# Optimization experiments

Measured on AMD Instinct MI355X. Metric: run time of the kernel, lower is better.

The kernel has to match this reference:

```python
import jax, jax.numpy as jnp
import numpy as np

SEQ, IN_DIM, OUT_DIM = 8192, 1024, 1024

def setup_inputs() -> dict:
    key = jax.random.key(0)
    k1, k2, k3, k4 = jax.random.split(key, 4)
    inputs = jax.random.normal(k1, (SEQ, IN_DIM), dtype=jnp.float32)
    # torch.nn.Linear stores weight as [out_dim, in_dim]; y = x @ W.T
    w_query = jax.random.normal(k2, (OUT_DIM, IN_DIM), dtype=jnp.float32) * (1.0 / np.sqrt(IN_DIM))
    w_key = jax.random.normal(k3, (OUT_DIM, IN_DIM), dtype=jnp.float32) * (1.0 / np.sqrt(IN_DIM))
    w_value = jax.random.normal(k4, (OUT_DIM, IN_DIM), dtype=jnp.float32) * (1.0 / np.sqrt(IN_DIM))
    return {"inputs": inputs, "w_query": w_query, "w_key": w_key, "w_value": w_value}

def reference(inputs, w_query, w_key, w_value):
    # QKV projections: [S, D_out]
    q = inputs @ w_query.T
    k = inputs @ w_key.T
    v = inputs @ w_value.T
    scale = 1.0 / jnp.sqrt(jnp.asarray(k.shape[-1], dtype=q.dtype))
    scores = (q @ k.T) * scale  # [S, S]
    # causal mask: lower-triangular kept, upper set to -inf
    s = scores.shape[0]
    causal = jnp.tril(jnp.ones((s, s), dtype=bool))
    scores = jnp.where(causal, scores, -jnp.inf)
    attn = jax.nn.softmax(scores, axis=-1)
    return attn @ v
```

## Files before the change

kernel.cpp:

```cpp
#include <hip/hip_runtime.h>
#include <stdint.h>
#include <stddef.h>


#define SEQ   8192
#define DIM   1024

typedef __bf16 bf16x8 __attribute__((ext_vector_type(8)));
typedef float  f32x4  __attribute__((ext_vector_type(4)));

#define MFMA16(a, b, c) __builtin_amdgcn_mfma_f32_16x16x32_bf16((a), (b), (c), 0, 0, 0)

__device__ __forceinline__ uint16_t f2bf(float f) {
  uint32_t u = __builtin_bit_cast(uint32_t, f);
  return (uint16_t)((u + 0x7fffu + ((u >> 16) & 1u)) >> 16);
}
__device__ __forceinline__ float bf2f(uint16_t h) {
  uint32_t u = ((uint32_t)h) << 16;
  return __builtin_bit_cast(float, u);
}

typedef const __attribute__((address_space(1))) uint32_t* gas_t;
typedef __attribute__((address_space(3))) uint32_t* las_t;
__device__ __forceinline__ void async16(const void* g, void* l) {
  __builtin_amdgcn_global_load_lds((gas_t)g, (las_t)l, 16, 0, 0);
}

__global__ __launch_bounds__(256) void cast_all(const float* __restrict__ x,
                                                const float* __restrict__ wq,
                                                const float* __restrict__ wk,
                                                const float* __restrict__ wv,
                                                uint16_t* __restrict__ xb,
                                                uint16_t* __restrict__ wcat) {
  int b = blockIdx.x;
  const float* src;
  uint16_t* dst;
  int i;
  if (b < 8192) {
    src = x; dst = xb; i = (b * 256 + threadIdx.x) * 4;
  } else {
    int wb = b - 8192;
    int sel = wb >> 10;
    src = sel == 0 ? wq : (sel == 1 ? wk : wv);
    dst = wcat + sel * 1048576;
    i = ((wb & 1023) * 256 + threadIdx.x) * 4;
  }
  float4 v = *(const float4*)(src + i);
  ushort4 o;
  o.x = f2bf(v.x); o.y = f2bf(v.y); o.z = f2bf(v.z); o.w = f2bf(v.w);
  *(ushort4*)(dst + i) = o;
}

__global__ __launch_bounds__(256) void qkv_gemm(const uint16_t* __restrict__ A,
                                                const uint16_t* __restrict__ B,
                                                uint16_t* __restrict__ Qblk,
                                                uint16_t* __restrict__ Kblk,
                                                uint16_t* __restrict__ Vblk) {
  __shared__ __align__(16) uint16_t As[128 * 64];
  __shared__ __align__(16) uint16_t Bs[128 * 64];
  const int t    = threadIdx.x;
  const int w    = t >> 6;
  const int lane = t & 63;
  const int lm   = lane & 15;
  const int qd   = lane >> 4;
  const int wrow = (w >> 1) * 64;
  const int wcol = (w & 1) * 64;
  const int rowbase = blockIdx.y * 128;
  const int colbase = blockIdx.x * 128;

  const int lrow = lane >> 3;
  const int lgrp = (lane & 7) ^ (lrow & 7);

  f32x4 acc[4][4] = {};

  for (int kb = 0; kb < DIM; kb += 64) {
    __syncthreads();
#pragma unroll
    for (int rep = 0; rep < 4; ++rep) {
      int r0 = rep * 32 + w * 8;
      async16(A + (size_t)(rowbase + r0 + lrow) * DIM + kb + lgrp * 8, As + r0 * 64);
      async16(B + (size_t)(colbase + r0 + lrow) * DIM + kb + lgrp * 8, Bs + r0 * 64);
    }
    __syncthreads();
#pragma unroll
    for (int kc = 0; kc < 2; ++kc) {
      bf16x8 af[4], bfr[4];
#pragma unroll
      for (int mt = 0; mt < 4; ++mt) {
        int r = wrow + mt * 16 + lm;
        af[mt] = *(const bf16x8*)(As + r * 64 + (((kc * 4 + qd) ^ (lm & 7)) * 8));
      }
#pragma unroll
      for (int nt = 0; nt < 4; ++nt) {
        int r = wcol + nt * 16 + lm;
        bfr[nt] = *(const bf16x8*)(Bs + r * 64 + (((kc * 4 + qd) ^ (lm & 7)) * 8));
      }
#pragma unroll
      for (int mt = 0; mt < 4; ++mt)
#pragma unroll
        for (int nt = 0; nt < 4; ++nt)
          acc[mt][nt] = MFMA16(af[mt], bfr[nt], acc[mt][nt]);
    }
  }

#pragma unroll
  for (int mt = 0; mt < 4; ++mt)
#pragma unroll
    for (int nt = 0; nt < 4; ++nt)
#pragma unroll
      for (int r = 0; r < 4; ++r) {
        int m = rowbase + wrow + mt * 16 + qd * 4 + r;
        int n = colbase + wcol + nt * 16 + lm;
        uint16_t v = f2bf(acc[mt][nt][r]);
        int nn = n & 1023;
        if (n < 2048) {
          size_t off = (((size_t)(m >> 4) * 32 + (nn >> 5)) * 64 +
                        ((nn >> 3) & 3) * 16 + (m & 15)) * 8 + (nn & 7);
          if (n < 1024) Qblk[off] = v; else Kblk[off] = v;
        } else {
          size_t off = (((size_t)(nn >> 4) * 256 + (m >> 5)) * 64 +
                        ((m >> 3) & 3) * 16 + (nn & 15)) * 8 + (m & 7);
          Vblk[off] = v;
        }
      }
}

__global__ __launch_bounds__(512, 2) void attn_kernel(const uint16_t* __restrict__ Qblk,
                                                      const uint16_t* __restrict__ Kblk,
                                                      const uint16_t* __restrict__ Vblk,
                                                      uint16_t* __restrict__ P0,
                                                      uint16_t* __restrict__ P1,
                                                      float* __restrict__ Mm,
                                                      float* __restrict__ Ll) {
  __shared__ __align__(16) uint16_t Qs[32768];
  __shared__ __align__(16) uint16_t Pb[8192];
  __shared__ float stats[32][8];
  __shared__ float mrow[32];

  const int t    = threadIdx.x;
  const int w    = t >> 6;
  const int lane = t & 63;
  const int lm   = lane & 15;
  const int qd   = lane >> 4;
  const int par  = blockIdx.x & 1;
  const int p    = blockIdx.x >> 1;
  const float c1 = 0.045084220027780106f;

#pragma unroll 1
  for (int half = 0; half < 2; ++half) {
    const int tt   = half ? 255 - p : p;
    const int row0 = tt * 32;
    const int jn   = (tt >> 3) + 1;

    __syncthreads();
#pragma unroll
    for (int i = 0; i < 8; ++i)
      async16(Qblk + ((size_t)(tt * 64 + w * 8 + i)) * 512 + lane * 8,
              Qs + (w * 8 + i) * 512);

    bf16x8 kpre0[4], kpre1[4];
    {
      const uint16_t* kbp0 = Kblk + ((size_t)(par * 16 + w * 2) * 32) * 512 + lane * 8;
#pragma unroll
      for (int c = 0; c < 4; ++c) {
        kpre0[c] = *(const bf16x8*)(kbp0 + (size_t)c * 512);
        kpre1[c] = *(const bf16x8*)(kbp0 + (size_t)(32 + c) * 512);
      }
    }
    __syncthreads();

    float m_run[2][4], l_run[2][4];
#pragma unroll
    for (int mt = 0; mt < 2; ++mt)
#pragma unroll
      for (int r = 0; r < 4; ++r) { m_run[mt][r] = -1e30f; l_run[mt][r] = 0.0f; }
    f32x4 o_acc[2][8] = {};

#pragma unroll 1
    for (int jg = par; jg < jn; jg += 2) {
      const uint16_t* kbp = Kblk + ((size_t)(jg * 16 + w * 2) * 32) * 512 + lane * 8;
      const uint16_t* vbp = Vblk + ((size_t)(w * 8) * 256 + jg * 8) * 512 + lane * 8;
      const uint16_t* qsp = Qs + lane * 8;

      f32x4 sacc[2][2] = {};
      bf16x8 kr0[8], kr1[8];
#pragma unroll
      for (int c = 0; c < 4; ++c) { kr0[c] = kpre0[c]; kr1[c] = kpre1[c]; }
#pragma unroll
      for (int c = 4; c < 8; ++c) {
        kr0[c] = *(const bf16x8*)(kbp + (size_t)c * 512);
        kr1[c] = *(const bf16x8*)(kbp + (size_t)(32 + c) * 512);
      }
#pragma unroll
      for (int kb = 0; kb < 32; ++kb) {
        bf16x8 q0 = *(const bf16x8*)(qsp + kb * 512);
        bf16x8 q1 = *(const bf16x8*)(qsp + (32 + kb) * 512);
        sacc[0][0] = MFMA16(q0, kr0[kb & 7], sacc[0][0]);
        sacc[1][0] = MFMA16(q1, kr0[kb & 7], sacc[1][0]);
        sacc[0][1] = MFMA16(q0, kr1[kb & 7], sacc[0][1]);
        sacc[1][1] = MFMA16(q1, kr1[kb & 7], sacc[1][1]);
        if (kb < 24) {
          kr0[kb & 7] = *(const bf16x8*)(kbp + (size_t)(kb + 8) * 512);
          kr1[kb & 7] = *(const bf16x8*)(kbp + (size_t)(32 + kb + 8) * 512);
        }
      }

      if (jg == jn - 1) {
#pragma unroll
        for (int mt = 0; mt < 2; ++mt)
#pragma unroll
          for (int nt = 0; nt < 2; ++nt)
#pragma unroll
            for (int r = 0; r < 4; ++r) {
              int col = jg * 256 + w * 32 + nt * 16 + lm;
              int row = row0 + mt * 16 + qd * 4 + r;
              if (col > row) sacc[mt][nt][r] = -1e30f;
            }
      }

#pragma unroll
      for (int mt = 0; mt < 2; ++mt)
#pragma unroll
        for (int r = 0; r < 4; ++r) {
          float v = fmaxf(sacc[mt][0][r], sacc[mt][1][r]);
          v = fmaxf(v, __shfl_xor(v, 1));
          v = fmaxf(v, __shfl_xor(v, 2));
          v = fmaxf(v, __shfl_xor(v, 4));
          v = fmaxf(v, __shfl_xor(v, 8));
          if (lm == 0) stats[mt * 16 + qd * 4 + r][w] = v;
        }
      __syncthreads();

      bf16x8 vr0[8], vr1[8];
#pragma unroll
      for (int dt = 0; dt < 8; ++dt) {
        vr0[dt] = *(const bf16x8*)(vbp + ((size_t)dt * 256 + 0) * 512);
        vr1[dt] = *(const bf16x8*)(vbp + ((size_t)dt * 256 + 1) * 512);
      }

      float alpha[2][4], psum[2][4];
#pragma unroll
      for (int mt = 0; mt < 2; ++mt)
#pragma unroll
        for (int r = 0; r < 4; ++r) {
          int rl = mt * 16 + qd * 4 + r;
          float4 g0 = *(const float4*)&stats[rl][0];
          float4 g1 = *(const float4*)&stats[rl][4];
          float gm = fmaxf(fmaxf(fmaxf(g0.x, g0.y), fmaxf(g0.z, g0.w)),
                           fmaxf(fmaxf(g1.x, g1.y), fmaxf(g1.z, g1.w)));
          float mn = fmaxf(m_run[mt][r], gm);
          alpha[mt][r] = exp2f((m_run[mt][r] - mn) * c1);
          m_run[mt][r] = mn;
          psum[mt][r] = 0.0f;
        }
#pragma unroll
      for (int mt = 0; mt < 2; ++mt)
#pragma unroll
        for (int nt = 0; nt < 2; ++nt)
#pragma unroll
          for (int r = 0; r < 4; ++r) {
            float pv = exp2f((sacc[mt][nt][r] - m_run[mt][r]) * c1);
            psum[mt][r] += pv;
            Pb[((mt * 8 + w) * 64 + (nt * 2 + (lm >> 3)) * 16 + qd * 4 + r) * 8 +
               (lm & 7)] = f2bf(pv);
          }
#pragma unroll
      for (int mt = 0; mt < 2; ++mt)
#pragma unroll
        for (int r = 0; r < 4; ++r) {
          float s2 = psum[mt][r];
          s2 += __shfl_xor(s2, 1);
          s2 += __shfl_xor(s2, 2);
          s2 += __shfl_xor(s2, 4);
          s2 += __shfl_xor(s2, 8);
          l_run[mt][r] = l_run[mt][r] * alpha[mt][r] + s2;
        }
      __syncthreads();

      {
        const uint16_t* kbpn = Kblk + ((size_t)((jg + 2) * 16 + w * 2) * 32) * 512 + lane * 8;
#pragma unroll
        for (int c = 0; c < 4; ++c) {
          kpre0[c] = *(const bf16x8*)(kbpn + (size_t)c * 512);
          kpre1[c] = *(const bf16x8*)(kbpn + (size_t)(32 + c) * 512);
        }
      }

#pragma unroll
      for (int mt = 0; mt < 2; ++mt)
#pragma unroll
        for (int dt = 0; dt < 8; ++dt)
#pragma unroll
          for (int r = 0; r < 4; ++r)
            o_acc[mt][dt][r] *= alpha[mt][r];

#pragma unroll
      for (int kc = 0; kc < 8; ++kc) {
        bf16x8 pf0 = *(const bf16x8*)(Pb + (kc * 64 + lane) * 8);
        bf16x8 pf1 = *(const bf16x8*)(Pb + ((8 + kc) * 64 + lane) * 8);
#pragma unroll
        for (int dt = 0; dt < 8; ++dt) {
          bf16x8 vf = (kc & 1) ? vr1[dt] : vr0[dt];
          o_acc[0][dt] = MFMA16(pf0, vf, o_acc[0][dt]);
          o_acc[1][dt] = MFMA16(pf1, vf, o_acc[1][dt]);
        }
        if (kc < 6) {
#pragma unroll
          for (int dt = 0; dt < 8; ++dt) {
            if (kc & 1)
              vr1[dt] = *(const bf16x8*)(vbp + ((size_t)dt * 256 + kc + 2) * 512);
            else
              vr0[dt] = *(const bf16x8*)(vbp + ((size_t)dt * 256 + kc + 2) * 512);
          }
        }
      }
    }

    if (lm == 0) {
#pragma unroll
      for (int mt = 0; mt < 2; ++mt)
#pragma unroll
        for (int r = 0; r < 4; ++r) {
          int rl = mt * 16 + qd * 4 + r;
          stats[rl][w] = l_run[mt][r];
          if (w == 0) mrow[rl] = m_run[mt][r];
        }
    }
    __syncthreads();
    if (t < 32) {
      float4 a0 = *(const float4*)&stats[t][0];
      float4 a1 = *(const float4*)&stats[t][4];
      Mm[par * SEQ + row0 + t] = mrow[t];
      Ll[par * SEQ + row0 + t] = (a0.x + a0.y + a0.z + a0.w) + (a1.x + a1.y + a1.z + a1.w);
    }
    uint16_t* Pp = par ? P1 : P0;
#pragma unroll
    for (int mt = 0; mt < 2; ++mt)
#pragma unroll
      for (int dt = 0; dt < 8; ++dt)
#pragma unroll
        for (int r = 0; r < 4; ++r) {
          int row = row0 + mt * 16 + qd * 4 + r;
          int d   = w * 128 + dt * 16 + lm;
          Pp[(size_t)row * DIM + d] = f2bf(o_acc[mt][dt][r]);
        }
  }
}

__global__ __launch_bounds__(256) void merge_kernel(const uint16_t* __restrict__ P0,
                                                    const uint16_t* __restrict__ P1,
                                                    const float* __restrict__ Mm,
                                                    const float* __restrict__ Ll,
                                                    float* __restrict__ out) {
  const int row = blockIdx.x;
  const int d0  = threadIdx.x * 4;
  const float c1 = 0.045084220027780106f;
  float m0 = Mm[row], m1 = Mm[SEQ + row];
  float l0 = Ll[row], l1 = Ll[SEQ + row];
  float m  = fmaxf(m0, m1);
  float a0 = exp2f((m0 - m) * c1);
  float a1 = exp2f((m1 - m) * c1);
  float inv = 1.0f / (a0 * l0 + a1 * l1);
  ushort4 p0 = *(const ushort4*)(P0 + (size_t)row * DIM + d0);
  ushort4 p1 = *(const ushort4*)(P1 + (size_t)row * DIM + d0);
  float4 o;
  o.x = (a0 * bf2f(p0.x) + a1 * bf2f(p1.x)) * inv;
  o.y = (a0 * bf2f(p0.y) + a1 * bf2f(p1.y)) * inv;
  o.z = (a0 * bf2f(p0.z) + a1 * bf2f(p1.z)) * inv;
  o.w = (a0 * bf2f(p0.w) + a1 * bf2f(p1.w)) * inv;
  *(float4*)(out + (size_t)row * DIM + d0) = o;
}

extern "C" void kernel_launch(void* const* d_in, const int* in_sizes, int n_in,
                              void* d_out, int out_size, void* d_ws, size_t ws_size,
                              hipStream_t stream) {
  (void)in_sizes; (void)n_in; (void)out_size; (void)ws_size;
  const float* x  = (const float*)d_in[0];
  const float* wq = (const float*)d_in[1];
  const float* wk = (const float*)d_in[2];
  const float* wv = (const float*)d_in[3];
  float* out = (float*)d_out;

  char* ws = (char*)d_ws;
  uint16_t* Qblk = (uint16_t*)(ws);
  uint16_t* Kblk = (uint16_t*)(ws + 16777216);
  uint16_t* Vblk = (uint16_t*)(ws + 33554432);
  uint16_t* P0   = (uint16_t*)(ws + 50331648);
  uint16_t* xb   = (uint16_t*)(ws + 67108864);
  uint16_t* P1   = (uint16_t*)(ws + 67108864);
  uint16_t* wcat = (uint16_t*)(ws + 83886080);
  float*    Mm   = (float*)(ws + 83886080);
  float*    Ll   = (float*)(ws + 83886080 + 65536);

  cast_all<<<11264, 256, 0, stream>>>(x, wq, wk, wv, xb, wcat);
  qkv_gemm<<<dim3(24, 64), 256, 0, stream>>>(xb, wcat, Qblk, Kblk, Vblk);
  attn_kernel<<<256, 512, 0, stream>>>(Qblk, Kblk, Vblk, P0, P1, Mm, Ll);
  merge_kernel<<<SEQ, 256, 0, stream>>>(P0, P1, Mm, Ll, out);
}
```

Before: 532.5 us.

## Launch one attention block per query tile and alias softmax stats into P buffer

The attention kernel no longer processes two query tiles (p and 255-p) in a loop per block. It now launches 512 blocks, each handling one tile and one key parity, and raises the launch-bounds occupancy hint from 2 to 4. The row-max and row-sum scratch arrays now reuse the P staging buffer in shared memory, which needs extra barriers. This aims for more concurrency and less idle time per block. The cost is losing the balanced pairing of light and heavy causal tiles, and the tighter register budget risks spills.

```diff
diff --git a/kernel.cpp b/kernel.cpp
--- a/kernel.cpp
+++ b/kernel.cpp
@@ -125,7 +125,7 @@
       }
 }
 
-__global__ __launch_bounds__(512, 2) void attn_kernel(const uint16_t* __restrict__ Qblk,
+__global__ __launch_bounds__(512, 4) void attn_kernel(const uint16_t* __restrict__ Qblk,
                                                       const uint16_t* __restrict__ Kblk,
                                                       const uint16_t* __restrict__ Vblk,
                                                       uint16_t* __restrict__ P0,
@@ -134,217 +134,224 @@
                                                       float* __restrict__ Ll) {
   __shared__ __align__(16) uint16_t Qs[32768];
   __shared__ __align__(16) uint16_t Pb[8192];
-  __shared__ float stats[32][8];
-  __shared__ float mrow[32];
+  float* const stats = (float*)Pb;
+  float* const mrow  = (float*)Pb + 256;
 
   const int t    = threadIdx.x;
   const int w    = t >> 6;
   const int lane = t & 63;
   const int lm   = lane & 15;
   const int qd   = lane >> 4;
-  const int par  = blockIdx.x & 1;
-  const int p    = blockIdx.x >> 1;
+  const int b    = blockIdx.x;
+  const int pi   = b >> 1;
+  const int par  = b & 1;
+  const int tt   = par ? 255 - pi : pi;
+  const int row0 = tt * 32;
+  const int jn   = (tt >> 3) + 1;
   const float c1 = 0.045084220027780106f;
 
+#pragma unroll
+  for (int i = 0; i < 8; ++i)
+    async16(Qblk + ((size_t)(tt * 64 + w * 8 + i)) * 512 + lane * 8,
+            Qs + (w * 8 + i) * 512);
+
+  bf16x8 kpre0[4], kpre1[4];
+  {
+    const uint16_t* kbp0 = Kblk + ((size_t)(par * 16 + w * 2) * 32) * 512 + lane * 8;
+#pragma unroll
+    for (int c = 0; c < 4; ++c) {
+      kpre0[c] = *(const bf16x8*)(kbp0 + (size_t)c * 512);
+      kpre1[c] = *(const bf16x8*)(kbp0 + (size_t)(32 + c) * 512);
+    }
+  }
+  __syncthreads();
+
+  float m_run[2][4], l_run[2][4];
+#pragma unroll
+  for (int mt = 0; mt < 2; ++mt)
+#pragma unroll
+    for (int r = 0; r < 4; ++r) { m_run[mt][r] = -1e30f; l_run[mt][r] = 0.0f; }
+  f32x4 o_acc[2][8] = {};
+
 #pragma unroll 1
-  for (int half = 0; half < 2; ++half) {
-    const int tt   = half ? 255 - p : p;
-    const int row0 = tt * 32;
-    const int jn   = (tt >> 3) + 1;
-
-    __syncthreads();
-#pragma unroll
-    for (int i = 0; i < 8; ++i)
-      async16(Qblk + ((size_t)(tt * 64 + w * 8 + i)) * 512 + lane * 8,
-              Qs + (w * 8 + i) * 512);
-
-    bf16x8 kpre0[4], kpre1[4];
+  for (int jg = par; jg < jn; jg += 2) {
+    const uint16_t* kbp = Kblk + ((size_t)(jg * 16 + w * 2) * 32) * 512 + lane * 8;
+    const uint16_t* vbp = Vblk + ((size_t)(w * 8) * 256 + jg * 8) * 512 + lane * 8;
+    const uint16_t* qsp = Qs + lane * 8;
+
+    f32x4 sacc[2][2] = {};
+    bf16x8 kr0[8], kr1[8];
+#pragma unroll
+    for (int c = 0; c < 4; ++c) { kr0[c] = kpre0[c]; kr1[c] = kpre1[c]; }
+#pragma unroll
+    for (int c = 4; c < 8; ++c) {
+      kr0[c] = *(const bf16x8*)(kbp + (size_t)c * 512);
+      kr1[c] = *(const bf16x8*)(kbp + (size_t)(32 + c) * 512);
+    }
+#pragma unroll
+    for (int kb = 0; kb < 32; ++kb) {
+      bf16x8 q0 = *(const bf16x8*)(qsp + kb * 512);
+      bf16x8 q1 = *(const bf16x8*)(qsp + (32 + kb) * 512);
+      sacc[0][0] = MFMA16(q0, kr0[kb & 7], sacc[0][0]);
+      sacc[1][0] = MFMA16(q1, kr0[kb & 7], sacc[1][0]);
+      sacc[0][1] = MFMA16(q0, kr1[kb & 7], sacc[0][1]);
+      sacc[1][1] = MFMA16(q1, kr1[kb & 7], sacc[1][1]);
+      if (kb < 24) {
+        kr0[kb & 7] = *(const bf16x8*)(kbp + (size_t)(kb + 8) * 512);
+        kr1[kb & 7] = *(const bf16x8*)(kbp + (size_t)(32 + kb + 8) * 512);
+      }
+    }
+
+    if (jg == jn - 1) {
+#pragma unroll
+      for (int mt = 0; mt < 2; ++mt)
+#pragma unroll
+        for (int nt = 0; nt < 2; ++nt)
+#pragma unroll
+          for (int r = 0; r < 4; ++r) {
+            int col = jg * 256 + w * 32 + nt * 16 + lm;
+            int row = row0 + mt * 16 + qd * 4 + r;
+            if (col > row) sacc[mt][nt][r] = -1e30f;
+          }
+    }
+
+    float rmax[2][4];
+#pragma unroll
+    for (int mt = 0; mt < 2; ++mt)
+#pragma unroll
+      for (int r = 0; r < 4; ++r) {
+        float v = fmaxf(sacc[mt][0][r], sacc[mt][1][r]);
+        v = fmaxf(v, __shfl_xor(v, 1));
+        v = fmaxf(v, __shfl_xor(v, 2));
+        v = fmaxf(v, __shfl_xor(v, 4));
+        v = fmaxf(v, __shfl_xor(v, 8));
+        rmax[mt][r] = v;
+      }
+    __syncthreads();
+
+#pragma unroll
+    for (int mt = 0; mt < 2; ++mt)
+#pragma unroll
+      for (int r = 0; r < 4; ++r)
+        if (lm == 0) stats[(mt * 16 + qd * 4 + r) * 8 + w] = rmax[mt][r];
+    __syncthreads();
+
+    float alpha[2][4], psum[2][4];
+#pragma unroll
+    for (int mt = 0; mt < 2; ++mt)
+#pragma unroll
+      for (int r = 0; r < 4; ++r) {
+        int rl = mt * 16 + qd * 4 + r;
+        float4 g0 = *(const float4*)&stats[rl * 8];
+        float4 g1 = *(const float4*)&stats[rl * 8 + 4];
+        float gm = fmaxf(fmaxf(fmaxf(g0.x, g0.y), fmaxf(g0.z, g0.w)),
+                         fmaxf(fmaxf(g1.x, g1.y), fmaxf(g1.z, g1.w)));
+        float mn = fmaxf(m_run[mt][r], gm);
+        alpha[mt][r] = exp2f((m_run[mt][r] - mn) * c1);
+        m_run[mt][r] = mn;
+        psum[mt][r] = 0.0f;
+      }
+    __syncthreads();
+
+    bf16x8 vr0[8], vr1[8];
+#pragma unroll
+    for (int dt = 0; dt < 8; ++dt) {
+      vr0[dt] = *(const bf16x8*)(vbp + ((size_t)dt * 256 + 0) * 512);
+      vr1[dt] = *(const bf16x8*)(vbp + ((size_t)dt * 256 + 1) * 512);
+    }
+
+#pragma unroll
+    for (int mt = 0; mt < 2; ++mt)
+#pragma unroll
+      for (int nt = 0; nt < 2; ++nt)
+#pragma unroll
+        for (int r = 0; r < 4; ++r) {
+          float pv = exp2f((sacc[mt][nt][r] - m_run[mt][r]) * c1);
+          psum[mt][r] += pv;
+          Pb[((mt * 8 + w) * 64 + (nt * 2 + (lm >> 3)) * 16 + qd * 4 + r) * 8 +
+             (lm & 7)] = f2bf(pv);
+        }
+#pragma unroll
+    for (int mt = 0; mt < 2; ++mt)
+#pragma unroll
+      for (int r = 0; r < 4; ++r) {
+        float s2 = psum[mt][r];
+        s2 += __shfl_xor(s2, 1);
+        s2 += __shfl_xor(s2, 2);
+        s2 += __shfl_xor(s2, 4);
+        s2 += __shfl_xor(s2, 8);
+        l_run[mt][r] = l_run[mt][r] * alpha[mt][r] + s2;
+      }
+    __syncthreads();
+
     {
-      const uint16_t* kbp0 = Kblk + ((size_t)(par * 16 + w * 2) * 32) * 512 + lane * 8;
+      const uint16_t* kbpn = Kblk + ((size_t)((jg + 2) * 16 + w * 2) * 32) * 512 + lane * 8;
 #pragma unroll
       for (int c = 0; c < 4; ++c) {
-        kpre0[c] = *(const bf16x8*)(kbp0 + (size_t)c * 512);
-        kpre1[c] = *(const bf16x8*)(kbp0 + (size_t)(32 + c) * 512);
-      }
-    }
-    __syncthreads();
-
-    float m_run[2][4], l_run[2][4];
-#pragma unroll
-    for (int mt = 0; mt < 2; ++mt)
-#pragma unroll
-      for (int r = 0; r < 4; ++r) { m_run[mt][r] = -1e30f; l_run[mt][r] = 0.0f; }
-    f32x4 o_acc[2][8] = {};
-
-#pragma unroll 1
-    for (int jg = par; jg < jn; jg += 2) {
-      const uint16_t* kbp = Kblk + ((size_t)(jg * 16 + w * 2) * 32) * 512 + lane * 8;
-      const uint16_t* vbp = Vblk + ((size_t)(w * 8) * 256 + jg * 8) * 512 + lane * 8;
-      const uint16_t* qsp = Qs + lane * 8;
-
-      f32x4 sacc[2][2] = {};
-      bf16x8 kr0[8], kr1[8];
-#pragma unroll
-      for (int c = 0; c < 4; ++c) { kr0[c] = kpre0[c]; kr1[c] = kpre1[c]; }
-#pragma unroll
-      for (int c = 4; c < 8; ++c) {
-        kr0[c] = *(const bf16x8*)(kbp + (size_t)c * 512);
-        kr1[c] = *(const bf16x8*)(kbp + (size_t)(32 + c) * 512);
-      }
-#pragma unroll
-      for (int kb = 0; kb < 32; ++kb) {
-        bf16x8 q0 = *(const bf16x8*)(qsp + kb * 512);
-        bf16x8 q1 = *(const bf16x8*)(qsp + (32 + kb) * 512);
-        sacc[0][0] = MFMA16(q0, kr0[kb & 7], sacc[0][0]);
-        sacc[1][0] = MFMA16(q1, kr0[kb & 7], sacc[1][0]);
-        sacc[0][1] = MFMA16(q0, kr1[kb & 7], sacc[0][1]);
-        sacc[1][1] = MFMA16(q1, kr1[kb & 7], sacc[1][1]);
-        if (kb < 24) {
-          kr0[kb & 7] = *(const bf16x8*)(kbp + (size_t)(kb + 8) * 512);
-          kr1[kb & 7] = *(const bf16x8*)(kbp + (size_t)(32 + kb + 8) * 512);
+        kpre0[c] = *(const bf16x8*)(kbpn + (size_t)c * 512);
+        kpre1[c] = *(const bf16x8*)(kbpn + (size_t)(32 + c) * 512);
+      }
+    }
+
+#pragma unroll
+    for (int mt = 0; mt < 2; ++mt)
+#pragma unroll
+      for (int dt = 0; dt < 8; ++dt)
+#pragma unroll
+        for (int r = 0; r < 4; ++r)
+          o_acc[mt][dt][r] *= alpha[mt][r];
+
+#pragma unroll
+    for (int kc = 0; kc < 8; ++kc) {
+      bf16x8 pf0 = *(const bf16x8*)(Pb + (kc * 64 + lane) * 8);
+      bf16x8 pf1 = *(const bf16x8*)(Pb + ((8 + kc) * 64 + lane) * 8);
+#pragma unroll
+      for (int dt = 0; dt < 8; ++dt) {
+        bf16x8 vf = (kc & 1) ? vr1[dt] : vr0[dt];
+        o_acc[0][dt] = MFMA16(pf0, vf, o_acc[0][dt]);
+        o_acc[1][dt] = MFMA16(pf1, vf, o_acc[1][dt]);
+      }
+      if (kc < 6) {
+#pragma unroll
+        for (int dt = 0; dt < 8; ++dt) {
+          if (kc & 1)
+            vr1[dt] = *(const bf16x8*)(vbp + ((size_t)dt * 256 + kc + 2) * 512);
+          else
+            vr0[dt] = *(const bf16x8*)(vbp + ((size_t)dt * 256 + kc + 2) * 512);
         }
       }
-
-      if (jg == jn - 1) {
-#pragma unroll
-        for (int mt = 0; mt < 2; ++mt)
-#pragma unroll
-          for (int nt = 0; nt < 2; ++nt)
-#pragma unroll
-            for (int r = 0; r < 4; ++r) {
-              int col = jg * 256 + w * 32 + nt * 16 + lm;
-              int row = row0 + mt * 16 + qd * 4 + r;
-              if (col > row) sacc[mt][nt][r] = -1e30f;
-            }
-      }
-
-#pragma unroll
-      for (int mt = 0; mt < 2; ++mt)
-#pragma unroll
-        for (int r = 0; r < 4; ++r) {
-          float v = fmaxf(sacc[mt][0][r], sacc[mt][1][r]);
-          v = fmaxf(v, __shfl_xor(v, 1));
-          v = fmaxf(v, __shfl_xor(v, 2));
-          v = fmaxf(v, __shfl_xor(v, 4));
-          v = fmaxf(v, __shfl_xor(v, 8));
-          if (lm == 0) stats[mt * 16 + qd * 4 + r][w] = v;
-        }
-      __syncthreads();
-
-      bf16x8 vr0[8], vr1[8];
-#pragma unroll
-      for (int dt = 0; dt < 8; ++dt) {
-        vr0[dt] = *(const bf16x8*)(vbp + ((size_t)dt * 256 + 0) * 512);
-        vr1[dt] = *(const bf16x8*)(vbp + ((size_t)dt * 256 + 1) * 512);
-      }
-
-      float alpha[2][4], psum[2][4];
-#pragma unroll
-      for (int mt = 0; mt < 2; ++mt)
-#pragma unroll
-        for (int r = 0; r < 4; ++r) {
-          int rl = mt * 16 + qd * 4 + r;
-          float4 g0 = *(const float4*)&stats[rl][0];
-          float4 g1 = *(const float4*)&stats[rl][4];
-          float gm = fmaxf(fmaxf(fmaxf(g0.x, g0.y), fmaxf(g0.z, g0.w)),
-                           fmaxf(fmaxf(g1.x, g1.y), fmaxf(g1.z, g1.w)));
-          float mn = fmaxf(m_run[mt][r], gm);
-          alpha[mt][r] = exp2f((m_run[mt][r] - mn) * c1);
-          m_run[mt][r] = mn;
-          psum[mt][r] = 0.0f;
-        }
-#pragma unroll
-      for (int mt = 0; mt < 2; ++mt)
-#pragma unroll
-        for (int nt = 0; nt < 2; ++nt)
-#pragma unroll
-          for (int r = 0; r < 4; ++r) {
-            float pv = exp2f((sacc[mt][nt][r] - m_run[mt][r]) * c1);
-            psum[mt][r] += pv;
-            Pb[((mt * 8 + w) * 64 + (nt * 2 + (lm >> 3)) * 16 + qd * 4 + r) * 8 +
-               (lm & 7)] = f2bf(pv);
-          }
-#pragma unroll
-      for (int mt = 0; mt < 2; ++mt)
-#pragma unroll
-        for (int r = 0; r < 4; ++r) {
-          float s2 = psum[mt][r];
-          s2 += __shfl_xor(s2, 1);
-          s2 += __shfl_xor(s2, 2);
-          s2 += __shfl_xor(s2, 4);
-          s2 += __shfl_xor(s2, 8);
-          l_run[mt][r] = l_run[mt][r] * alpha[mt][r] + s2;
-        }
-      __syncthreads();
-
-      {
-        const uint16_t* kbpn = Kblk + ((size_t)((jg + 2) * 16 + w * 2) * 32) * 512 + lane * 8;
-#pragma unroll
-        for (int c = 0; c < 4; ++c) {
-          kpre0[c] = *(const bf16x8*)(kbpn + (size_t)c * 512);
-          kpre1[c] = *(const bf16x8*)(kbpn + (size_t)(32 + c) * 512);
-        }
-      }
-
-#pragma unroll
-      for (int mt = 0; mt < 2; ++mt)
-#pragma unroll
-        for (int dt = 0; dt < 8; ++dt)
-#pragma unroll
-          for (int r = 0; r < 4; ++r)
-            o_acc[mt][dt][r] *= alpha[mt][r];
-
-#pragma unroll
-      for (int kc = 0; kc < 8; ++kc) {
-        bf16x8 pf0 = *(const bf16x8*)(Pb + (kc * 64 + lane) * 8);
-        bf16x8 pf1 = *(const bf16x8*)(Pb + ((8 + kc) * 64 + lane) * 8);
-#pragma unroll
-        for (int dt = 0; dt < 8; ++dt) {
-          bf16x8 vf = (kc & 1) ? vr1[dt] : vr0[dt];
-          o_acc[0][dt] = MFMA16(pf0, vf, o_acc[0][dt]);
-          o_acc[1][dt] = MFMA16(pf1, vf, o_acc[1][dt]);
-        }
-        if (kc < 6) {
-#pragma unroll
-          for (int dt = 0; dt < 8; ++dt) {
-            if (kc & 1)
-              vr1[dt] = *(const bf16x8*)(vbp + ((size_t)dt * 256 + kc + 2) * 512);
-            else
-              vr0[dt] = *(const bf16x8*)(vbp + ((size_t)dt * 256 + kc + 2) * 512);
-          }
-        }
-      }
-    }
-
-    if (lm == 0) {
-#pragma unroll
-      for (int mt = 0; mt < 2; ++mt)
-#pragma unroll
-        for (int r = 0; r < 4; ++r) {
-          int rl = mt * 16 + qd * 4 + r;
-          stats[rl][w] = l_run[mt][r];
-          if (w == 0) mrow[rl] = m_run[mt][r];
-        }
-    }
-    __syncthreads();
-    if (t < 32) {
-      float4 a0 = *(const float4*)&stats[t][0];
-      float4 a1 = *(const float4*)&stats[t][4];
-      Mm[par * SEQ + row0 + t] = mrow[t];
-      Ll[par * SEQ + row0 + t] = (a0.x + a0.y + a0.z + a0.w) + (a1.x + a1.y + a1.z + a1.w);
-    }
-    uint16_t* Pp = par ? P1 : P0;
-#pragma unroll
-    for (int mt = 0; mt < 2; ++mt)
-#pragma unroll
-      for (int dt = 0; dt < 8; ++dt)
-#pragma unroll
-        for (int r = 0; r < 4; ++r) {
-          int row = row0 + mt * 16 + qd * 4 + r;
-          int d   = w * 128 + dt * 16 + lm;
-          Pp[(size_t)row * DIM + d] = f2bf(o_acc[mt][dt][r]);
-        }
-  }
+    }
+  }
+
+  __syncthreads();
+  if (lm == 0) {
+#pragma unroll
+    for (int mt = 0; mt < 2; ++mt)
+#pragma unroll
+      for (int r = 0; r < 4; ++r) {
+        int rl = mt * 16 + qd * 4 + r;
+        stats[rl * 8 + w] = l_run[mt][r];
+        if (w == 0) mrow[rl] = m_run[mt][r];
+      }
+  }
+  __syncthreads();
+  if (t < 32) {
+    float4 a0 = *(const float4*)&stats[t * 8];
+    float4 a1 = *(const float4*)&stats[t * 8 + 4];
+    Mm[par * SEQ + row0 + t] = mrow[t];
+    Ll[par * SEQ + row0 + t] = (a0.x + a0.y + a0.z + a0.w) + (a1.x + a1.y + a1.z + a1.w);
+  }
+  uint16_t* Pp = par ? P1 : P0;
+#pragma unroll
+  for (int mt = 0; mt < 2; ++mt)
+#pragma unroll
+    for (int dt = 0; dt < 8; ++dt)
+#pragma unroll
+      for (int r = 0; r < 4; ++r) {
+        int row = row0 + mt * 16 + qd * 4 + r;
+        int d   = w * 128 + dt * 16 + lm;
+        Pp[(size_t)row * DIM + d] = f2bf(o_acc[mt][dt][r]);
+      }
 }
 
 __global__ __launch_bounds__(256) void merge_kernel(const uint16_t* __restrict__ P0,
@@ -394,6 +401,6 @@
 
   cast_all<<<11264, 256, 0, stream>>>(x, wq, wk, wv, xb, wcat);
   qkv_gemm<<<dim3(24, 64), 256, 0, stream>>>(xb, wcat, Qblk, Kblk, Vblk);
-  attn_kernel<<<256, 512, 0, stream>>>(Qblk, Kblk, Vblk, P0, P1, Mm, Ll);
+  attn_kernel<<<512, 512, 0, stream>>>(Qblk, Kblk, Vblk, P0, P1, Mm, Ll);
   merge_kernel<<<SEQ, 256, 0, stream>>>(P0, P1, Mm, Ll, out);
 }
```

Measured after the change: 839.4 us. 57.6% more time.

## Split attention work across 16 waves per block instead of 8

Applied to the files above, without the earlier changes.

Doubles the attention block to 1024 threads, so each wave handles a 16-column slice of the key block and a 64-wide slice of the output dimension, which halves per-wave registers and accumulators. The stats array widens to 16 waves, the P tile layout is remapped, and the second V register set is loaded later to shorten its live range. The aim is more waves in flight per CU to hide memory and MFMA latency with the same 256-block grid. The cost is more barrier participants, more redundant Q reads from LDS per MFMA, and a larger cross-wave max reduction.

```diff
diff --git a/kernel.cpp b/kernel.cpp
--- a/kernel.cpp
+++ b/kernel.cpp
@@ -125,16 +125,16 @@
       }
 }
 
-__global__ __launch_bounds__(512, 2) void attn_kernel(const uint16_t* __restrict__ Qblk,
-                                                      const uint16_t* __restrict__ Kblk,
-                                                      const uint16_t* __restrict__ Vblk,
-                                                      uint16_t* __restrict__ P0,
-                                                      uint16_t* __restrict__ P1,
-                                                      float* __restrict__ Mm,
-                                                      float* __restrict__ Ll) {
+__global__ __launch_bounds__(1024) void attn_kernel(const uint16_t* __restrict__ Qblk,
+                                                    const uint16_t* __restrict__ Kblk,
+                                                    const uint16_t* __restrict__ Vblk,
+                                                    uint16_t* __restrict__ P0,
+                                                    uint16_t* __restrict__ P1,
+                                                    float* __restrict__ Mm,
+                                                    float* __restrict__ Ll) {
   __shared__ __align__(16) uint16_t Qs[32768];
   __shared__ __align__(16) uint16_t Pb[8192];
-  __shared__ float stats[32][8];
+  __shared__ float stats[32][16];
   __shared__ float mrow[32];
 
   const int t    = threadIdx.x;
@@ -154,18 +154,16 @@
 
     __syncthreads();
 #pragma unroll
-    for (int i = 0; i < 8; ++i)
-      async16(Qblk + ((size_t)(tt * 64 + w * 8 + i)) * 512 + lane * 8,
-              Qs + (w * 8 + i) * 512);
-
-    bf16x8 kpre0[4], kpre1[4];
+    for (int i = 0; i < 4; ++i)
+      async16(Qblk + ((size_t)(tt * 64 + w * 4 + i)) * 512 + lane * 8,
+              Qs + (w * 4 + i) * 512);
+
+    bf16x8 kpre[4];
     {
-      const uint16_t* kbp0 = Kblk + ((size_t)(par * 16 + w * 2) * 32) * 512 + lane * 8;
-#pragma unroll
-      for (int c = 0; c < 4; ++c) {
-        kpre0[c] = *(const bf16x8*)(kbp0 + (size_t)c * 512);
-        kpre1[c] = *(const bf16x8*)(kbp0 + (size_t)(32 + c) * 512);
-      }
+      const uint16_t* kbp0 = Kblk + ((size_t)(par * 16 + w) * 32) * 512 + lane * 8;
+#pragma unroll
+      for (int c = 0; c < 4; ++c)
+        kpre[c] = *(const bf16x8*)(kbp0 + (size_t)c * 512);
     }
     __syncthreads();
 
@@ -174,55 +172,47 @@
     for (int mt = 0; mt < 2; ++mt)
 #pragma unroll
       for (int r = 0; r < 4; ++r) { m_run[mt][r] = -1e30f; l_run[mt][r] = 0.0f; }
-    f32x4 o_acc[2][8] = {};
+    f32x4 o_acc[2][4] = {};
 
 #pragma unroll 1
     for (int jg = par; jg < jn; jg += 2) {
-      const uint16_t* kbp = Kblk + ((size_t)(jg * 16 + w * 2) * 32) * 512 + lane * 8;
-      const uint16_t* vbp = Vblk + ((size_t)(w * 8) * 256 + jg * 8) * 512 + lane * 8;
+      const uint16_t* kbp = Kblk + ((size_t)(jg * 16 + w) * 32) * 512 + lane * 8;
+      const uint16_t* vbp = Vblk + ((size_t)(w * 4) * 256 + jg * 8) * 512 + lane * 8;
       const uint16_t* qsp = Qs + lane * 8;
 
-      f32x4 sacc[2][2] = {};
-      bf16x8 kr0[8], kr1[8];
-#pragma unroll
-      for (int c = 0; c < 4; ++c) { kr0[c] = kpre0[c]; kr1[c] = kpre1[c]; }
-#pragma unroll
-      for (int c = 4; c < 8; ++c) {
-        kr0[c] = *(const bf16x8*)(kbp + (size_t)c * 512);
-        kr1[c] = *(const bf16x8*)(kbp + (size_t)(32 + c) * 512);
-      }
+      f32x4 sacc[2] = {};
+      bf16x8 kr[8];
+#pragma unroll
+      for (int c = 0; c < 4; ++c) kr[c] = kpre[c];
+#pragma unroll
+      for (int c = 4; c < 8; ++c)
+        kr[c] = *(const bf16x8*)(kbp + (size_t)c * 512);
 #pragma unroll
       for (int kb = 0; kb < 32; ++kb) {
         bf16x8 q0 = *(const bf16x8*)(qsp + kb * 512);
         bf16x8 q1 = *(const bf16x8*)(qsp + (32 + kb) * 512);
-        sacc[0][0] = MFMA16(q0, kr0[kb & 7], sacc[0][0]);
-        sacc[1][0] = MFMA16(q1, kr0[kb & 7], sacc[1][0]);
-        sacc[0][1] = MFMA16(q0, kr1[kb & 7], sacc[0][1]);
-        sacc[1][1] = MFMA16(q1, kr1[kb & 7], sacc[1][1]);
-        if (kb < 24) {
-          kr0[kb & 7] = *(const bf16x8*)(kbp + (size_t)(kb + 8) * 512);
-          kr1[kb & 7] = *(const bf16x8*)(kbp + (size_t)(32 + kb + 8) * 512);
-        }
+        sacc[0] = MFMA16(q0, kr[kb & 7], sacc[0]);
+        sacc[1] = MFMA16(q1, kr[kb & 7], sacc[1]);
+        if (kb < 24)
+          kr[kb & 7] = *(const bf16x8*)(kbp + (size_t)(kb + 8) * 512);
       }
 
       if (jg == jn - 1) {
 #pragma unroll
         for (int mt = 0; mt < 2; ++mt)
 #pragma unroll
-          for (int nt = 0; nt < 2; ++nt)
-#pragma unroll
-            for (int r = 0; r < 4; ++r) {
-              int col = jg * 256 + w * 32 + nt * 16 + lm;
-              int row = row0 + mt * 16 + qd * 4 + r;
-              if (col > row) sacc[mt][nt][r] = -1e30f;
-            }
-      }
-
-#pragma unroll
-      for (int mt = 0; mt < 2; ++mt)
-#pragma unroll
-        for (int r = 0; r < 4; ++r) {
-          float v = fmaxf(sacc[mt][0][r], sacc[mt][1][r]);
+          for (int r = 0; r < 4; ++r) {
+            int col = jg * 256 + w * 16 + lm;
+            int row = row0 + mt * 16 + qd * 4 + r;
+            if (col > row) sacc[mt][r] = -1e30f;
+          }
+      }
+
+#pragma unroll
+      for (int mt = 0; mt < 2; ++mt)
+#pragma unroll
+        for (int r = 0; r < 4; ++r) {
+          float v = sacc[mt][r];
           v = fmaxf(v, __shfl_xor(v, 1));
           v = fmaxf(v, __shfl_xor(v, 2));
           v = fmaxf(v, __shfl_xor(v, 4));
@@ -231,12 +221,10 @@
         }
       __syncthreads();
 
-      bf16x8 vr0[8], vr1[8];
-#pragma unroll
-      for (int dt = 0; dt < 8; ++dt) {
+      bf16x8 vr0[4], vr1[4];
+#pragma unroll
+      for (int dt = 0; dt < 4; ++dt)
         vr0[dt] = *(const bf16x8*)(vbp + ((size_t)dt * 256 + 0) * 512);
-        vr1[dt] = *(const bf16x8*)(vbp + ((size_t)dt * 256 + 1) * 512);
-      }
 
       float alpha[2][4], psum[2][4];
 #pragma unroll
@@ -246,8 +234,13 @@
           int rl = mt * 16 + qd * 4 + r;
           float4 g0 = *(const float4*)&stats[rl][0];
           float4 g1 = *(const float4*)&stats[rl][4];
-          float gm = fmaxf(fmaxf(fmaxf(g0.x, g0.y), fmaxf(g0.z, g0.w)),
-                           fmaxf(fmaxf(g1.x, g1.y), fmaxf(g1.z, g1.w)));
+          float4 g2 = *(const float4*)&stats[rl][8];
+          float4 g3 = *(const float4*)&stats[rl][12];
+          float gm = fmaxf(
+              fmaxf(fmaxf(fmaxf(g0.x, g0.y), fmaxf(g0.z, g0.w)),
+                    fmaxf(fmaxf(g1.x, g1.y), fmaxf(g1.z, g1.w))),
+              fmaxf(fmaxf(fmaxf(g2.x, g2.y), fmaxf(g2.z, g2.w)),
+                    fmaxf(fmaxf(g3.x, g3.y), fmaxf(g3.z, g3.w))));
           float mn = fmaxf(m_run[mt][r], gm);
           alpha[mt][r] = exp2f((m_run[mt][r] - mn) * c1);
           m_run[mt][r] = mn;
@@ -256,14 +249,17 @@
 #pragma unroll
       for (int mt = 0; mt < 2; ++mt)
 #pragma unroll
-        for (int nt = 0; nt < 2; ++nt)
-#pragma unroll
-          for (int r = 0; r < 4; ++r) {
-            float pv = exp2f((sacc[mt][nt][r] - m_run[mt][r]) * c1);
-            psum[mt][r] += pv;
-            Pb[((mt * 8 + w) * 64 + (nt * 2 + (lm >> 3)) * 16 + qd * 4 + r) * 8 +
-               (lm & 7)] = f2bf(pv);
-          }
+        for (int r = 0; r < 4; ++r) {
+          float pv = exp2f((sacc[mt][r] - m_run[mt][r]) * c1);
+          psum[mt][r] += pv;
+          Pb[((mt * 8 + (w >> 1)) * 64 + ((w & 1) * 2 + (lm >> 3)) * 16 +
+              qd * 4 + r) * 8 + (lm & 7)] = f2bf(pv);
+        }
+
+#pragma unroll
+      for (int dt = 0; dt < 4; ++dt)
+        vr1[dt] = *(const bf16x8*)(vbp + ((size_t)dt * 256 + 1) * 512);
+
 #pragma unroll
       for (int mt = 0; mt < 2; ++mt)
 #pragma unroll
@@ -278,18 +274,16 @@
       __syncthreads();
 
       {
-        const uint16_t* kbpn = Kblk + ((size_t)((jg + 2) * 16 + w * 2) * 32) * 512 + lane * 8;
-#pragma unroll
-        for (int c = 0; c < 4; ++c) {
-          kpre0[c] = *(const bf16x8*)(kbpn + (size_t)c * 512);
-          kpre1[c] = *(const bf16x8*)(kbpn + (size_t)(32 + c) * 512);
-        }
-      }
-
-#pragma unroll
-      for (int mt = 0; mt < 2; ++mt)
-#pragma unroll
-        for (int dt = 0; dt < 8; ++dt)
+        const uint16_t* kbpn = Kblk + ((size_t)((jg + 2) * 16 + w) * 32) * 512 + lane * 8;
+#pragma unroll
+        for (int c = 0; c < 4; ++c)
+          kpre[c] = *(const bf16x8*)(kbpn + (size_t)c * 512);
+      }
+
+#pragma unroll
+      for (int mt = 0; mt < 2; ++mt)
+#pragma unroll
+        for (int dt = 0; dt < 4; ++dt)
 #pragma unroll
           for (int r = 0; r < 4; ++r)
             o_acc[mt][dt][r] *= alpha[mt][r];
@@ -299,14 +293,14 @@
         bf16x8 pf0 = *(const bf16x8*)(Pb + (kc * 64 + lane) * 8);
         bf16x8 pf1 = *(const bf16x8*)(Pb + ((8 + kc) * 64 + lane) * 8);
 #pragma unroll
-        for (int dt = 0; dt < 8; ++dt) {
+        for (int dt = 0; dt < 4; ++dt) {
           bf16x8 vf = (kc & 1) ? vr1[dt] : vr0[dt];
           o_acc[0][dt] = MFMA16(pf0, vf, o_acc[0][dt]);
           o_acc[1][dt] = MFMA16(pf1, vf, o_acc[1][dt]);
         }
         if (kc < 6) {
 #pragma unroll
-          for (int dt = 0; dt < 8; ++dt) {
+          for (int dt = 0; dt < 4; ++dt) {
             if (kc & 1)
               vr1[dt] = *(const bf16x8*)(vbp + ((size_t)dt * 256 + kc + 2) * 512);
             else
@@ -330,18 +324,23 @@
     if (t < 32) {
       float4 a0 = *(const float4*)&stats[t][0];
       float4 a1 = *(const float4*)&stats[t][4];
+      float4 a2 = *(const float4*)&stats[t][8];
+      float4 a3 = *(const float4*)&stats[t][12];
       Mm[par * SEQ + row0 + t] = mrow[t];
-      Ll[par * SEQ + row0 + t] = (a0.x + a0.y + a0.z + a0.w) + (a1.x + a1.y + a1.z + a1.w);
+      Ll[par * SEQ + row0 + t] = (a0.x + a0.y + a0.z + a0.w) +
+                                 (a1.x + a1.y + a1.z + a1.w) +
+                                 (a2.x + a2.y + a2.z + a2.w) +
+                                 (a3.x + a3.y + a3.z + a3.w);
     }
     uint16_t* Pp = par ? P1 : P0;
 #pragma unroll
     for (int mt = 0; mt < 2; ++mt)
 #pragma unroll
-      for (int dt = 0; dt < 8; ++dt)
+      for (int dt = 0; dt < 4; ++dt)
 #pragma unroll
         for (int r = 0; r < 4; ++r) {
           int row = row0 + mt * 16 + qd * 4 + r;
-          int d   = w * 128 + dt * 16 + lm;
+          int d   = w * 64 + dt * 16 + lm;
           Pp[(size_t)row * DIM + d] = f2bf(o_acc[mt][dt][r]);
         }
   }
@@ -394,6 +393,6 @@
 
   cast_all<<<11264, 256, 0, stream>>>(x, wq, wk, wv, xb, wcat);
   qkv_gemm<<<dim3(24, 64), 256, 0, stream>>>(xb, wcat, Qblk, Kblk, Vblk);
-  attn_kernel<<<256, 512, 0, stream>>>(Qblk, Kblk, Vblk, P0, P1, Mm, Ll);
+  attn_kernel<<<256, 1024, 0, stream>>>(Qblk, Kblk, Vblk, P0, P1, Mm, Ll);
   merge_kernel<<<SEQ, 256, 0, stream>>>(P0, P1, Mm, Ll, out);
 }
```

Result: no change. 535.9 us (+0.6%).
